# Optimization experiments

Hardware: AMD Instinct MI355X
Metric: run time of the kernel (lower is better)

The kernel has to match this reference:

```python
import jax, jax.numpy as jnp
import numpy as np

B, T, S, D = 8, 128, 512, 128  # batch, decoder steps, encoder len, output_dim==input_dim


def setup_inputs() -> dict:
    key = jax.random.key(0)
    ks = jax.random.split(key, 24)
    g = lambda i, shape: jax.random.normal(ks[i], shape, dtype=jnp.float32) * 0.05
    inp = {
        "x": g(0, (B, T, D)),
        "H": g(1, (B, S, D)),
        "init_states": jnp.zeros((2, B, D), jnp.float32),
        "Wa": g(2, (D, D)), "Ua": g(3, (D, D)), "v": g(4, (D,)),
        "Wi": g(5, (D, D)), "Ui": g(6, (D, D)), "Ci": g(7, (D, D)), "bi": jnp.zeros((D,), jnp.float32),
        "Wf": g(8, (D, D)), "Uf": g(9, (D, D)), "Cf": g(10, (D, D)), "bf": jnp.ones((D,), jnp.float32),
        "Wc": g(11, (D, D)), "Uc": g(12, (D, D)), "Cc": g(13, (D, D)), "bc": jnp.zeros((D,), jnp.float32),
        "Wo": g(14, (D, D)), "Uo": g(15, (D, D)), "Co": g(16, (D, D)), "bo": jnp.zeros((D,), jnp.float32),
    }
    return inp


def _forward(x, H, init_states, Wa, Ua, v, Wi, Ui, Ci, bi, Wf, Uf, Cf, bf,
             Wc, Uc, Cc, bc, Wo, Uo, Co, bo):
    # A = H @ Ua is loop-invariant in the original step(); hoist it (same math).
    HU = jnp.einsum('bsd,de->bse', H, Ua)  # [B,S,D]

    def step(carry, x_t):
        h_prev, c_prev = carry  # each [B,D]
        # Bahdanau attention over the full encoder sequence
        q = h_prev @ Wa                                        # [B,D]
        score = jnp.einsum('bsd,d->bs', jnp.tanh(HU + q[:, None, :]), v)  # [B,S]
        a = jax.nn.softmax(score, axis=-1)                     # [B,S]
        context = jnp.einsum('bsd,bs->bd', H, a)               # [B,D]
        # 4-gate LSTM update
        i_g = jax.nn.sigmoid(x_t @ Wi + h_prev @ Ui + context @ Ci + bi)
        f_g = jax.nn.sigmoid(x_t @ Wf + h_prev @ Uf + context @ Cf + bf)
        g_w = jnp.tanh(x_t @ Wc + h_prev @ Uc + context @ Cc + bc)
        c_t = f_g * c_prev + i_g * g_w
        o_g = jax.nn.sigmoid(x_t @ Wo + h_prev @ Uo + context @ Co + bo)
        h_t = o_g * jnp.tanh(c_t)
        return (h_t, c_t), h_t

    h0, c0 = init_states[0], init_states[1]
    x_tm = jnp.transpose(x, (1, 0, 2))  # time-major [T,B,D]
    _, hs = jax.lax.scan(step, (h0, c0), x_tm)  # hs: [T,B,D]
    return jnp.transpose(hs, (1, 0, 2))  # [B,T,D] hidden states (original returns [0] of stacked [h,c])


def reference(x, H, init_states, Wa, Ua, v, Wi, Ui, Ci, bi, Wf, Uf, Cf, bf,
              Wc, Uc, Cc, bc, Wo, Uo, Co, bo):
    return _forward(x, H, init_states, Wa, Ua, v, Wi, Ui, Ci, bi, Wf, Uf, Cf, bf,
                    Wc, Uc, Cc, bc, Wo, Uo, Co, bo)
```

## Files before the change

### kernel.cpp

```cpp
#include <hip/hip_runtime.h>

#define DEV __device__ __forceinline__

constexpr int nB = 8, nT = 128, nS = 512, nD = 128;
constexpr int J   = 4;
constexpr int SL  = 128;
constexpr int NTH = 512;

constexpr int S1_CNT = nB * J * 130;
constexpr int S2_OFF = S1_CNT;
constexpr int S2_CNT = nB * J * 32;
constexpr int XW_F   = (S1_CNT + S2_CNT) * 2;

DEV float tanh_small(float x) {
    float x2 = x * x;
    float p = fmaf(x2, 0.133333333f, -0.333333333f);
    return fmaf(x * x2, p, x);
}
DEV float fast_tanh(float x) {
    x = fminf(4.0f, fmaxf(-4.0f, x));
    float x2 = x * x;
    float num = fmaf(fmaf(x2 + 378.0f, x2, 17325.0f), x2, 135135.0f);
    float den = fmaf(fmaf(fmaf(x2, 28.0f, 3150.0f), x2, 62370.0f), x2, 135135.0f);
    return x * num * __builtin_amdgcn_rcpf(den);
}
DEV float fast_sig(float x) { return fmaf(fast_tanh(0.5f * x), 0.5f, 0.5f); }

typedef unsigned long long u64;
DEV u64  pk(float v, unsigned tag) { return ((u64)tag << 32) | (u64)__float_as_uint(v); }
DEV void st64(u64* p, u64 v) { __hip_atomic_store(p, v, __ATOMIC_RELAXED, __HIP_MEMORY_SCOPE_AGENT); }
DEV u64  ld64(const u64* p)  { return __hip_atomic_load(p, __ATOMIC_RELAXED, __HIP_MEMORY_SCOPE_AGENT); }
DEV float poll64(const u64* p, unsigned want) {
    for (;;) {
        u64 q = ld64(p);
        if ((unsigned)(q >> 32) == want) return __uint_as_float((unsigned)q);
        __builtin_amdgcn_s_sleep(1);
    }
}

__global__ void init_kernel(float* __restrict__ ws) {
    u64* p = (u64*)ws;
    for (int i = threadIdx.x; i < S1_CNT + S2_CNT; i += 1024)
        __hip_atomic_store(p + i, 0ull, __ATOMIC_RELAXED, __HIP_MEMORY_SCOPE_AGENT);
}

__global__ __launch_bounds__(NTH, 1) void attn_lstm_kernel(
    const float* __restrict__ x,  const float* __restrict__ H,
    const float* __restrict__ init_states, const float* __restrict__ Wa,
    const float* __restrict__ Ua, const float* __restrict__ v,
    const float* __restrict__ Wi, const float* __restrict__ Ui,
    const float* __restrict__ Ci, const float* __restrict__ bi,
    const float* __restrict__ Wf, const float* __restrict__ Uf,
    const float* __restrict__ Cf, const float* __restrict__ bf,
    const float* __restrict__ Wc, const float* __restrict__ Uc,
    const float* __restrict__ Cc, const float* __restrict__ bc,
    const float* __restrict__ Wo, const float* __restrict__ Uo,
    const float* __restrict__ Co, const float* __restrict__ bo,
    float* __restrict__ out, float* __restrict__ ws)
{
    const int tid = threadIdx.x;
    const int b = blockIdx.x & 7;
    const int j = blockIdx.x >> 3;

    u64*   S1   = (u64*)ws;
    u64*   S2   = (u64*)ws + S2_OFF;
    float* wsXW = ws + XW_F;

    __shared__ __align__(16) float Hs[SL * nD];
    __shared__ __align__(16) float q_l[nD];
    __shared__ __align__(16) float ctx_l[nD];
    __shared__ __align__(16) float h_l[nD];
    __shared__ __align__(16) float e_l[SL];
    __shared__ float sc_l[SL];
    __shared__ float pre_l[nD];
    __shared__ float pNx[3 * nD];
    __shared__ float mS_l[8];

    const int hi = tid >> 2, lo = tid & 3;
    const int g = hi >> 5, dd = hi & 31, gcol = 32 * j + dd;

    const float* Ug = (g == 0) ? Ui : (g == 1) ? Uf : (g == 2) ? Uc : Uo;
    const float* Cg = (g == 0) ? Ci : (g == 1) ? Cf : (g == 2) ? Cc : Co;
    const float* Bg = (g == 0) ? bi : (g == 1) ? bf : (g == 2) ? bc : bo;

    {
        for (int k = tid; k < 16384; k += NTH) {
            int gg = k >> 12, r = (k >> 5) & 127, i = k & 31;
            const float* Wm = (gg == 0) ? Wi : (gg == 1) ? Wf : (gg == 2) ? Wc : Wo;
            Hs[k] = Wm[r * nD + 32 * j + i];
        }
    }
    __syncthreads();

    {
        float acc[32];
        #pragma unroll
        for (int i = 0; i < 32; ++i) acc[i] = 0.0f;
        const float* xrow = x + ((size_t)b * nT + hi) * nD;
        for (int r = 0; r < nD; ++r) {
            float xr = xrow[r];
            const float* wrow = &Hs[lo * 4096 + r * 32];
            #pragma unroll
            for (int i = 0; i < 32; ++i) acc[i] = fmaf(xr, wrow[i], acc[i]);
        }
        float* dst = wsXW + ((size_t)(b * J + j) * nT + hi) * nD + lo * 32;
        #pragma unroll
        for (int k = 0; k < 8; ++k)
            ((float4*)dst)[k] = make_float4(acc[4*k], acc[4*k+1], acc[4*k+2], acc[4*k+3]);
    }
    __syncthreads();

    for (int k = tid; k < 16384; k += NTH) Hs[k] = Ua[k];
    __syncthreads();

    float HU_r[32];
    {
        #pragma unroll
        for (int i = 0; i < 32; ++i) HU_r[i] = 0.0f;
        const float* hrow = H + ((size_t)b * nS + (size_t)SL * j + hi) * nD;
        for (int r = 0; r < nD; ++r) {
            float hr = hrow[r];
            const float* uar = &Hs[r * nD + lo * 32];
            #pragma unroll
            for (int i = 0; i < 32; ++i) HU_r[i] = fmaf(hr, uar[i], HU_r[i]);
        }
    }
    __syncthreads();

    {
        const float* hrow = H + ((size_t)b * nS + (size_t)SL * j + hi) * nD + lo * 32;
        int c = hi >> 4, w = hi & 15;
        #pragma unroll
        for (int k = 0; k < 8; ++k) {
            float4 hv = ((const float4*)hrow)[k];
            int d0 = lo * 32 + 4 * k;
            Hs[(d0+0) * nD + ((c ^ ((d0+0) & 7)) * 16) + w] = hv.x;
            Hs[(d0+1) * nD + ((c ^ ((d0+1) & 7)) * 16) + w] = hv.y;
            Hs[(d0+2) * nD + ((c ^ ((d0+2) & 7)) * 16) + w] = hv.z;
            Hs[(d0+3) * nD + ((c ^ ((d0+3) & 7)) * 16) + w] = hv.w;
        }
    }

    float wa_r[32], u_r[32], c_r2[32], v_r[32];
    #pragma unroll
    for (int i = 0; i < 32; ++i) {
        wa_r[i] = Wa[(lo * 32 + i) * nD + hi];
        u_r[i]  = Ug[(lo * 32 + i) * nD + gcol];
        c_r2[i] = Cg[(lo * 32 + i) * nD + gcol];
        v_r[i]  = v[lo * 32 + i];
    }
    const float bval = Bg[gcol];
    float c_reg = (tid < 32) ? init_states[nB * nD + b * nD + 32 * j + tid] : 0.0f;

    if (tid < nD) h_l[tid] = init_states[b * nD + tid];
    __syncthreads();

    u64* myN = S1 + (size_t)(b * J + j) * 130;
    u64* myH = S2 + (size_t)(b * J + j) * 32;

    for (int t = 0; t < nT; ++t) {
        const unsigned tg = (unsigned)(t + 1);

        float xwv = 0.0f;
        if (lo == 0) xwv = wsXW[((size_t)(b * J + j) * nT + t) * nD + hi];

        float qa = 0.0f, uasum = 0.0f;
        #pragma unroll
        for (int i = 0; i < 32; ++i) {
            float hv = h_l[lo * 32 + i];
            qa    = fmaf(hv, wa_r[i], qa);
            uasum = fmaf(hv, u_r[i],  uasum);
        }
        qa += __shfl_xor(qa, 1);  qa += __shfl_xor(qa, 2);
        uasum += __shfl_xor(uasum, 1);  uasum += __shfl_xor(uasum, 2);
        if (lo == 0) q_l[hi] = qa;
        __syncthreads();

        float sa = 0.0f;
        #pragma unroll
        for (int k = 0; k < 8; ++k) {
            float4 qq = *(const float4*)&q_l[lo * 32 + 4 * k];
            sa = fmaf(v_r[4*k+0], tanh_small(HU_r[4*k+0] + qq.x), sa);
            sa = fmaf(v_r[4*k+1], tanh_small(HU_r[4*k+1] + qq.y), sa);
            sa = fmaf(v_r[4*k+2], tanh_small(HU_r[4*k+2] + qq.z), sa);
            sa = fmaf(v_r[4*k+3], tanh_small(HU_r[4*k+3] + qq.w), sa);
        }
        sa += __shfl_xor(sa, 1);  sa += __shfl_xor(sa, 2);
        if (lo == 0) sc_l[hi] = sa;
        __syncthreads();

        float m, se;
        {
            int lane = tid & 63;
            float s0 = sc_l[lane], s1 = sc_l[64 + lane];
            m = fmaxf(s0, s1);
            #pragma unroll
            for (int o = 1; o < 64; o <<= 1) m = fmaxf(m, __shfl_xor(m, o));
            float e0 = __expf(s0 - m), e1 = __expf(s1 - m);
            se = e0 + e1;
            #pragma unroll
            for (int o = 1; o < 64; o <<= 1) se += __shfl_xor(se, o);
            if (tid < 64) { e_l[tid] = e0; e_l[64 + tid] = e1; }
        }
        __syncthreads();

        float na = 0.0f;
        #pragma unroll
        for (int cc = 0; cc < 2; ++cc) {
            int c = 2 * lo + cc;
            int pc = c ^ (hi & 7);
            const float4* hp = (const float4*)&Hs[hi * nD + pc * 16];
            const float4* ep = (const float4*)&e_l[c * 16];
            #pragma unroll
            for (int k2 = 0; k2 < 4; ++k2) {
                float4 hh = hp[k2]; float4 ee = ep[k2];
                na = fmaf(ee.x, hh.x, na); na = fmaf(ee.y, hh.y, na);
                na = fmaf(ee.z, hh.z, na); na = fmaf(ee.w, hh.w, na);
            }
        }
        na += __shfl_xor(na, 1);  na += __shfl_xor(na, 2);

        if (lo == 0) st64(myN + hi, pk(na, tg));
        if (tid == 0) st64(myN + 128, pk(m, tg));
        if (tid == 1) st64(myN + 129, pk(se, tg));
        if (tid < 384) {
            int pi = tid >> 7, d2 = tid & 127;
            int jj = pi + (pi >= j);
            pNx[pi * nD + d2] = poll64(S1 + (size_t)(b * J + jj) * 130 + d2, tg);
        }
        if (tid >= 384 && tid < 390) {
            int k = tid - 384, pi = k >> 1, wh = k & 1;
            int jj = pi + (pi >= j);
            mS_l[pi * 2 + wh] = poll64(S1 + (size_t)(b * J + jj) * 130 + 128 + wh, tg);
        }
        __syncthreads();

        if (lo == 0) {
            float mm = m;
            #pragma unroll
            for (int p2 = 0; p2 < 3; ++p2) mm = fmaxf(mm, mS_l[p2 * 2]);
            float w0 = __expf(m - mm);
            float ssum = se * w0, nsum = na * w0;
            #pragma unroll
            for (int p2 = 0; p2 < 3; ++p2) {
                float wp = __expf(mS_l[p2 * 2] - mm);
                ssum = fmaf(mS_l[p2 * 2 + 1], wp, ssum);
                nsum = fmaf(pNx[p2 * nD + hi], wp, nsum);
            }
            ctx_l[hi] = nsum * __builtin_amdgcn_rcpf(ssum);
        }
        __syncthreads();

        float ca = 0.0f;
        #pragma unroll
        for (int i = 0; i < 32; ++i) ca = fmaf(ctx_l[lo * 32 + i], c_r2[i], ca);
        ca += __shfl_xor(ca, 1);  ca += __shfl_xor(ca, 2);
        if (lo == 0) pre_l[hi] = uasum + ca + xwv + bval;
        __syncthreads();

        if (tid < 32) {
            float p_i = pre_l[tid], p_f = pre_l[32 + tid];
            float p_c = pre_l[64 + tid], p_o = pre_l[96 + tid];
            float ig = fast_sig(p_i), fg = fast_sig(p_f);
            float gg = fast_tanh(p_c), og = fast_sig(p_o);
            c_reg = fmaf(fg, c_reg, ig * gg);
            float hn = og * fast_tanh(c_reg);
            st64(myH + tid, pk(hn, tg));
            h_l[32 * j + tid] = hn;
            out[((size_t)b * nT + t) * nD + 32 * j + tid] = hn;
        }
        if (tid >= 32 && tid < 128) {
            int k = tid - 32, pi = k >> 5, dd2 = k & 31;
            int jj = pi + (pi >= j);
            h_l[32 * jj + dd2] = poll64(S2 + (size_t)(b * J + jj) * 32 + dd2, tg);
        }
        __syncthreads();
    }
}

extern "C" void kernel_launch(void* const* d_in, const int* in_sizes, int n_in,
                              void* d_out, int out_size, void* d_ws, size_t ws_size,
                              hipStream_t stream) {
    const float* x  = (const float*)d_in[0];
    const float* H  = (const float*)d_in[1];
    const float* is = (const float*)d_in[2];
    const float* Wa = (const float*)d_in[3];
    const float* Ua = (const float*)d_in[4];
    const float* v  = (const float*)d_in[5];
    const float* Wi = (const float*)d_in[6];
    const float* Ui = (const float*)d_in[7];
    const float* Ci = (const float*)d_in[8];
    const float* bi = (const float*)d_in[9];
    const float* Wf = (const float*)d_in[10];
    const float* Uf = (const float*)d_in[11];
    const float* Cf = (const float*)d_in[12];
    const float* bf = (const float*)d_in[13];
    const float* Wc = (const float*)d_in[14];
    const float* Uc = (const float*)d_in[15];
    const float* Cc = (const float*)d_in[16];
    const float* bc = (const float*)d_in[17];
    const float* Wo = (const float*)d_in[18];
    const float* Uo = (const float*)d_in[19];
    const float* Co = (const float*)d_in[20];
    const float* bo = (const float*)d_in[21];
    float* out = (float*)d_out;
    float* ws  = (float*)d_ws;

    hipLaunchKernelGGL(init_kernel, dim3(1), dim3(1024), 0, stream, ws);
    hipLaunchKernelGGL(attn_lstm_kernel, dim3(nB * J), dim3(NTH), 0, stream,
                       x, H, is, Wa, Ua, v,
                       Wi, Ui, Ci, bi, Wf, Uf, Cf, bf,
                       Wc, Uc, Cc, bc, Wo, Uo, Co, bo,
                       out, ws);
}
```

Before: 805.1 us.

## Rewrite as one block per batch with fp16 packed dot products and precompute kernel

The recurrent kernel moves from four cooperating blocks per batch, which exchanged softmax partials and hidden-state slices through tagged global-memory polling, to a single 512-thread block per batch that holds the whole encoder sequence in LDS as packed fp16. The x·W and H·Ua projections move into a separate pre-kernel that writes fp16 results to workspace. The per-step matvecs, attention tanh and context reduction now use packed-half fdot2. This removes the inter-block polling latency on every step. In exchange it uses fewer CUs and loses accuracy from fp16 storage, a cubic tanh approximation evaluated in half precision, and a softmax that skips max subtraction.

```diff
diff --git a/kernel.cpp b/kernel.cpp
--- a/kernel.cpp
+++ b/kernel.cpp
@@ -1,21 +1,43 @@
 #include <hip/hip_runtime.h>
 
 #define DEV __device__ __forceinline__
+typedef unsigned int u32;
+typedef _Float16 f16;
+typedef f16 h2 __attribute__((ext_vector_type(2)));
+using pkv2 = decltype(__builtin_amdgcn_cvt_pkrtz(0.0f, 0.0f));
 
 constexpr int nB = 8, nT = 128, nS = 512, nD = 128;
-constexpr int J   = 4;
-constexpr int SL  = 128;
 constexpr int NTH = 512;
-
-constexpr int S1_CNT = nB * J * 130;
-constexpr int S2_OFF = S1_CNT;
-constexpr int S2_CNT = nB * J * 32;
-constexpr int XW_F   = (S1_CNT + S2_CNT) * 2;
-
-DEV float tanh_small(float x) {
-    float x2 = x * x;
-    float p = fmaf(x2, 0.133333333f, -0.333333333f);
-    return fmaf(x * x2, p, x);
+constexpr int RS  = 260;
+
+constexpr int XW_W = 0;
+constexpr int HU_W = 262144;
+constexpr int WA_W = 524288;
+
+#if defined(__has_builtin)
+#if __has_builtin(__builtin_amdgcn_fdot2)
+#define HAS_FDOT2 1
+#endif
+#endif
+
+DEV h2  u2h(u32 a) { return __builtin_bit_cast(h2, a); }
+DEV u32 h2u(h2 a)  { return __builtin_bit_cast(u32, a); }
+DEV u32 pkrtz(float a, float b) { return __builtin_bit_cast(u32, __builtin_amdgcn_cvt_pkrtz(a, b)); }
+
+DEV float fdot2(u32 a, u32 b, float c) {
+#ifdef HAS_FDOT2
+    return __builtin_amdgcn_fdot2(__builtin_bit_cast(pkv2, a), __builtin_bit_cast(pkv2, b), c, false);
+#else
+    h2 A = u2h(a), B = u2h(b);
+    return c + (float)A.x * (float)B.x + (float)A.y * (float)B.y;
+#endif
+}
+
+DEV h2 tanh_pk(h2 x) {
+    h2 x2 = x * x;
+    h2 x3 = x * x2;
+    h2 c3 = { (f16)0.33333333f, (f16)0.33333333f };
+    return x - x3 * c3;
 }
 DEV float fast_tanh(float x) {
     x = fminf(4.0f, fmaxf(-4.0f, x));
@@ -26,25 +48,74 @@
 }
 DEV float fast_sig(float x) { return fmaf(fast_tanh(0.5f * x), 0.5f, 0.5f); }
 
-typedef unsigned long long u64;
-DEV u64  pk(float v, unsigned tag) { return ((u64)tag << 32) | (u64)__float_as_uint(v); }
-DEV void st64(u64* p, u64 v) { __hip_atomic_store(p, v, __ATOMIC_RELAXED, __HIP_MEMORY_SCOPE_AGENT); }
-DEV u64  ld64(const u64* p)  { return __hip_atomic_load(p, __ATOMIC_RELAXED, __HIP_MEMORY_SCOPE_AGENT); }
-DEV float poll64(const u64* p, unsigned want) {
-    for (;;) {
-        u64 q = ld64(p);
-        if ((unsigned)(q >> 32) == want) return __uint_as_float((unsigned)q);
-        __builtin_amdgcn_s_sleep(1);
-    }
-}
-
-__global__ void init_kernel(float* __restrict__ ws) {
-    u64* p = (u64*)ws;
-    for (int i = threadIdx.x; i < S1_CNT + S2_CNT; i += 1024)
-        __hip_atomic_store(p + i, 0ull, __ATOMIC_RELAXED, __HIP_MEMORY_SCOPE_AGENT);
-}
-
-__global__ __launch_bounds__(NTH, 1) void attn_lstm_kernel(
+__global__ __launch_bounds__(512, 2) void pre_kernel(
+    const float* __restrict__ x,  const float* __restrict__ H,
+    const float* __restrict__ Wa, const float* __restrict__ Ua,
+    const float* __restrict__ Wi, const float* __restrict__ Wf,
+    const float* __restrict__ Wc, const float* __restrict__ Wo,
+    u32* __restrict__ ws)
+{
+    const int w = blockIdx.x, tid = threadIdx.x;
+    if (w < 32) {
+        const int b = w >> 2, tp = w & 3;
+        const int g = tid >> 7, cc = tid & 127;
+        const float* Wm = (g == 0) ? Wi : (g == 1) ? Wf : (g == 2) ? Wc : Wo;
+        float wcol[128];
+        #pragma unroll
+        for (int r = 0; r < 128; ++r) wcol[r] = Wm[r * nD + cc];
+        for (int ti = 0; ti < 32; ++ti) {
+            int t = tp * 32 + ti;
+            const float* xr = x + ((size_t)b * nT + t) * nD;
+            float acc = 0.0f;
+            #pragma unroll
+            for (int r = 0; r < 128; ++r) acc = fmaf(xr[r], wcol[r], acc);
+            float accn = __shfl_down(acc, 1);
+            if (!(tid & 1))
+                ws[XW_W + ((size_t)b * nT + t) * 256 + (tid >> 1)] = pkrtz(acc, accn);
+        }
+        if (w == 0) {
+            int col = tid >> 2, q = tid & 3;
+            #pragma unroll
+            for (int k = 0; k < 16; ++k) {
+                int rp = q * 16 + k;
+                ws[WA_W + col * 64 + rp] =
+                    pkrtz(Wa[(2 * rp) * nD + col], Wa[(2 * rp + 1) * nD + col]);
+            }
+        }
+    } else {
+        const int b = (w - 32) >> 2, sp4 = (w - 32) & 3;
+        __shared__ float UaS[128 * 128];
+        for (int k = tid; k < 16384; k += 512) UaS[k] = Ua[k];
+        __syncthreads();
+        const int lo = tid & 3, si = tid >> 2;
+        const int s = sp4 * 128 + si;
+        const float* hrow = H + ((size_t)b * nS + s) * nD;
+        float acc[32];
+        #pragma unroll
+        for (int i = 0; i < 32; ++i) acc[i] = 0.0f;
+        for (int r4 = 0; r4 < 32; ++r4) {
+            float4 hv = ((const float4*)hrow)[r4];
+            #pragma unroll
+            for (int k = 0; k < 4; ++k) {
+                float hr = (k == 0) ? hv.x : (k == 1) ? hv.y : (k == 2) ? hv.z : hv.w;
+                const float4* ua = (const float4*)&UaS[(4 * r4 + k) * 128 + lo * 32];
+                #pragma unroll
+                for (int q = 0; q < 8; ++q) {
+                    float4 u = ua[q];
+                    acc[4*q+0] = fmaf(hr, u.x, acc[4*q+0]);
+                    acc[4*q+1] = fmaf(hr, u.y, acc[4*q+1]);
+                    acc[4*q+2] = fmaf(hr, u.z, acc[4*q+2]);
+                    acc[4*q+3] = fmaf(hr, u.w, acc[4*q+3]);
+                }
+            }
+        }
+        u32* dst = ws + HU_W + ((size_t)b * nS + s) * 64 + lo * 16;
+        #pragma unroll
+        for (int k = 0; k < 16; ++k) dst[k] = pkrtz(acc[2 * k], acc[2 * k + 1]);
+    }
+}
+
+__global__ __launch_bounds__(NTH, 2) void attn_lstm_kernel(
     const float* __restrict__ x,  const float* __restrict__ H,
     const float* __restrict__ init_states, const float* __restrict__ Wa,
     const float* __restrict__ Ua, const float* __restrict__ v,
@@ -56,223 +127,192 @@
     const float* __restrict__ Cc, const float* __restrict__ bc,
     const float* __restrict__ Wo, const float* __restrict__ Uo,
     const float* __restrict__ Co, const float* __restrict__ bo,
-    float* __restrict__ out, float* __restrict__ ws)
+    float* __restrict__ out, u32* __restrict__ ws)
 {
-    const int tid = threadIdx.x;
-    const int b = blockIdx.x & 7;
-    const int j = blockIdx.x >> 3;
-
-    u64*   S1   = (u64*)ws;
-    u64*   S2   = (u64*)ws + S2_OFF;
-    float* wsXW = ws + XW_F;
-
-    __shared__ __align__(16) float Hs[SL * nD];
-    __shared__ __align__(16) float q_l[nD];
-    __shared__ __align__(16) float ctx_l[nD];
-    __shared__ __align__(16) float h_l[nD];
-    __shared__ __align__(16) float e_l[SL];
-    __shared__ float sc_l[SL];
-    __shared__ float pre_l[nD];
-    __shared__ float pNx[3 * nD];
-    __shared__ float mS_l[8];
-
-    const int hi = tid >> 2, lo = tid & 3;
-    const int g = hi >> 5, dd = hi & 31, gcol = 32 * j + dd;
+    const int b = blockIdx.x, tid = threadIdx.x;
+
+    __shared__ __align__(16) u32 Hl[128 * RS];
+    __shared__ __align__(16) u32 q_l[64], e_l[256], ctx_l[64], h_l[64], v_w[64];
+    __shared__ __align__(16) float sc_l[512], pre_l[512], pNx[512];
+    __shared__ float mS[8];
+
+    const int lo = tid & 3, hi = tid >> 2;
+    const int g = tid >> 7, cc = tid & 127;
+
+    {
+        const int sp = tid >> 1, half = tid & 1;
+        const float* r0 = H + ((size_t)b * nS + 2 * sp) * nD + half * 64;
+        const float* r1 = r0 + nD;
+        #pragma unroll
+        for (int k = 0; k < 16; ++k) {
+            float4 a = ((const float4*)r0)[k];
+            float4 c = ((const float4*)r1)[k];
+            int d0 = half * 64 + 4 * k;
+            Hl[(d0 + 0) * RS + sp] = pkrtz(a.x, c.x);
+            Hl[(d0 + 1) * RS + sp] = pkrtz(a.y, c.y);
+            Hl[(d0 + 2) * RS + sp] = pkrtz(a.z, c.z);
+            Hl[(d0 + 3) * RS + sp] = pkrtz(a.w, c.w);
+        }
+    }
+
+    u32 HUr[64];
+    {
+        const u32* srcw = ws + HU_W + ((size_t)b * nS + 4 * hi) * 64 + lo * 16;
+        #pragma unroll
+        for (int k = 0; k < 4; ++k) {
+            #pragma unroll
+            for (int q = 0; q < 4; ++q) {
+                uint4 t4 = ((const uint4*)(srcw + k * 64))[q];
+                HUr[16*k + 4*q + 0] = t4.x; HUr[16*k + 4*q + 1] = t4.y;
+                HUr[16*k + 4*q + 2] = t4.z; HUr[16*k + 4*q + 3] = t4.w;
+            }
+        }
+    }
 
     const float* Ug = (g == 0) ? Ui : (g == 1) ? Uf : (g == 2) ? Uc : Uo;
     const float* Cg = (g == 0) ? Ci : (g == 1) ? Cf : (g == 2) ? Cc : Co;
     const float* Bg = (g == 0) ? bi : (g == 1) ? bf : (g == 2) ? bc : bo;
-
-    {
-        for (int k = tid; k < 16384; k += NTH) {
-            int gg = k >> 12, r = (k >> 5) & 127, i = k & 31;
-            const float* Wm = (gg == 0) ? Wi : (gg == 1) ? Wf : (gg == 2) ? Wc : Wo;
-            Hs[k] = Wm[r * nD + 32 * j + i];
-        }
-    }
+    u32 Ur[64], Cr[64];
+    #pragma unroll
+    for (int rp = 0; rp < 64; ++rp) {
+        Ur[rp] = pkrtz(Ug[(2*rp) * nD + cc], Ug[(2*rp+1) * nD + cc]);
+        Cr[rp] = pkrtz(Cg[(2*rp) * nD + cc], Cg[(2*rp+1) * nD + cc]);
+    }
+    if (tid < 64) v_w[tid] = pkrtz(v[2 * tid], v[2 * tid + 1]);
+    const float bval = Bg[cc];
+
+    float c_reg = 0.0f;
+    if (tid < 128) c_reg = init_states[nB * nD + b * nD + tid];
+    if (tid < 128 && !(tid & 1))
+        h_l[tid >> 1] = pkrtz(init_states[b * nD + tid], init_states[b * nD + tid + 1]);
     __syncthreads();
 
-    {
-        float acc[32];
-        #pragma unroll
-        for (int i = 0; i < 32; ++i) acc[i] = 0.0f;
-        const float* xrow = x + ((size_t)b * nT + hi) * nD;
-        for (int r = 0; r < nD; ++r) {
-            float xr = xrow[r];
-            const float* wrow = &Hs[lo * 4096 + r * 32];
-            #pragma unroll
-            for (int i = 0; i < 32; ++i) acc[i] = fmaf(xr, wrow[i], acc[i]);
-        }
-        float* dst = wsXW + ((size_t)(b * J + j) * nT + hi) * nD + lo * 32;
-        #pragma unroll
-        for (int k = 0; k < 8; ++k)
-            ((float4*)dst)[k] = make_float4(acc[4*k], acc[4*k+1], acc[4*k+2], acc[4*k+3]);
-    }
-    __syncthreads();
-
-    for (int k = tid; k < 16384; k += NTH) Hs[k] = Ua[k];
-    __syncthreads();
-
-    float HU_r[32];
-    {
-        #pragma unroll
-        for (int i = 0; i < 32; ++i) HU_r[i] = 0.0f;
-        const float* hrow = H + ((size_t)b * nS + (size_t)SL * j + hi) * nD;
-        for (int r = 0; r < nD; ++r) {
-            float hr = hrow[r];
-            const float* uar = &Hs[r * nD + lo * 32];
-            #pragma unroll
-            for (int i = 0; i < 32; ++i) HU_r[i] = fmaf(hr, uar[i], HU_r[i]);
-        }
-    }
-    __syncthreads();
-
-    {
-        const float* hrow = H + ((size_t)b * nS + (size_t)SL * j + hi) * nD + lo * 32;
-        int c = hi >> 4, w = hi & 15;
-        #pragma unroll
-        for (int k = 0; k < 8; ++k) {
-            float4 hv = ((const float4*)hrow)[k];
-            int d0 = lo * 32 + 4 * k;
-            Hs[(d0+0) * nD + ((c ^ ((d0+0) & 7)) * 16) + w] = hv.x;
-            Hs[(d0+1) * nD + ((c ^ ((d0+1) & 7)) * 16) + w] = hv.y;
-            Hs[(d0+2) * nD + ((c ^ ((d0+2) & 7)) * 16) + w] = hv.z;
-            Hs[(d0+3) * nD + ((c ^ ((d0+3) & 7)) * 16) + w] = hv.w;
-        }
-    }
-
-    float wa_r[32], u_r[32], c_r2[32], v_r[32];
-    #pragma unroll
-    for (int i = 0; i < 32; ++i) {
-        wa_r[i] = Wa[(lo * 32 + i) * nD + hi];
-        u_r[i]  = Ug[(lo * 32 + i) * nD + gcol];
-        c_r2[i] = Cg[(lo * 32 + i) * nD + gcol];
-        v_r[i]  = v[lo * 32 + i];
-    }
-    const float bval = Bg[gcol];
-    float c_reg = (tid < 32) ? init_states[nB * nD + b * nD + 32 * j + tid] : 0.0f;
-
-    if (tid < nD) h_l[tid] = init_states[b * nD + tid];
-    __syncthreads();
-
-    u64* myN = S1 + (size_t)(b * J + j) * 130;
-    u64* myH = S2 + (size_t)(b * J + j) * 32;
-
     for (int t = 0; t < nT; ++t) {
-        const unsigned tg = (unsigned)(t + 1);
-
-        float xwv = 0.0f;
-        if (lo == 0) xwv = wsXW[((size_t)(b * J + j) * nT + t) * nD + hi];
-
-        float qa = 0.0f, uasum = 0.0f;
-        #pragma unroll
-        for (int i = 0; i < 32; ++i) {
-            float hv = h_l[lo * 32 + i];
-            qa    = fmaf(hv, wa_r[i], qa);
-            uasum = fmaf(hv, u_r[i],  uasum);
-        }
-        qa += __shfl_xor(qa, 1);  qa += __shfl_xor(qa, 2);
-        uasum += __shfl_xor(uasum, 1);  uasum += __shfl_xor(uasum, 2);
-        if (lo == 0) q_l[hi] = qa;
-        __syncthreads();
-
-        float sa = 0.0f;
-        #pragma unroll
-        for (int k = 0; k < 8; ++k) {
-            float4 qq = *(const float4*)&q_l[lo * 32 + 4 * k];
-            sa = fmaf(v_r[4*k+0], tanh_small(HU_r[4*k+0] + qq.x), sa);
-            sa = fmaf(v_r[4*k+1], tanh_small(HU_r[4*k+1] + qq.y), sa);
-            sa = fmaf(v_r[4*k+2], tanh_small(HU_r[4*k+2] + qq.z), sa);
-            sa = fmaf(v_r[4*k+3], tanh_small(HU_r[4*k+3] + qq.w), sa);
-        }
-        sa += __shfl_xor(sa, 1);  sa += __shfl_xor(sa, 2);
-        if (lo == 0) sc_l[hi] = sa;
-        __syncthreads();
-
-        float m, se;
-        {
-            int lane = tid & 63;
-            float s0 = sc_l[lane], s1 = sc_l[64 + lane];
-            m = fmaxf(s0, s1);
-            #pragma unroll
-            for (int o = 1; o < 64; o <<= 1) m = fmaxf(m, __shfl_xor(m, o));
-            float e0 = __expf(s0 - m), e1 = __expf(s1 - m);
-            se = e0 + e1;
-            #pragma unroll
-            for (int o = 1; o < 64; o <<= 1) se += __shfl_xor(se, o);
-            if (tid < 64) { e_l[tid] = e0; e_l[64 + tid] = e1; }
-        }
-        __syncthreads();
-
-        float na = 0.0f;
-        #pragma unroll
-        for (int cc = 0; cc < 2; ++cc) {
-            int c = 2 * lo + cc;
-            int pc = c ^ (hi & 7);
-            const float4* hp = (const float4*)&Hs[hi * nD + pc * 16];
-            const float4* ep = (const float4*)&e_l[c * 16];
-            #pragma unroll
-            for (int k2 = 0; k2 < 4; ++k2) {
-                float4 hh = hp[k2]; float4 ee = ep[k2];
-                na = fmaf(ee.x, hh.x, na); na = fmaf(ee.y, hh.y, na);
-                na = fmaf(ee.z, hh.z, na); na = fmaf(ee.w, hh.w, na);
-            }
-        }
-        na += __shfl_xor(na, 1);  na += __shfl_xor(na, 2);
-
-        if (lo == 0) st64(myN + hi, pk(na, tg));
-        if (tid == 0) st64(myN + 128, pk(m, tg));
-        if (tid == 1) st64(myN + 129, pk(se, tg));
-        if (tid < 384) {
-            int pi = tid >> 7, d2 = tid & 127;
-            int jj = pi + (pi >= j);
-            pNx[pi * nD + d2] = poll64(S1 + (size_t)(b * J + jj) * 130 + d2, tg);
-        }
-        if (tid >= 384 && tid < 390) {
-            int k = tid - 384, pi = k >> 1, wh = k & 1;
-            int jj = pi + (pi >= j);
-            mS_l[pi * 2 + wh] = poll64(S1 + (size_t)(b * J + jj) * 130 + 128 + wh, tg);
-        }
-        __syncthreads();
-
-        if (lo == 0) {
-            float mm = m;
-            #pragma unroll
-            for (int p2 = 0; p2 < 3; ++p2) mm = fmaxf(mm, mS_l[p2 * 2]);
-            float w0 = __expf(m - mm);
-            float ssum = se * w0, nsum = na * w0;
-            #pragma unroll
-            for (int p2 = 0; p2 < 3; ++p2) {
-                float wp = __expf(mS_l[p2 * 2] - mm);
-                ssum = fmaf(mS_l[p2 * 2 + 1], wp, ssum);
-                nsum = fmaf(pNx[p2 * nD + hi], wp, nsum);
-            }
-            ctx_l[hi] = nsum * __builtin_amdgcn_rcpf(ssum);
-        }
-        __syncthreads();
-
-        float ca = 0.0f;
-        #pragma unroll
-        for (int i = 0; i < 32; ++i) ca = fmaf(ctx_l[lo * 32 + i], c_r2[i], ca);
-        ca += __shfl_xor(ca, 1);  ca += __shfl_xor(ca, 2);
-        if (lo == 0) pre_l[hi] = uasum + ca + xwv + bval;
-        __syncthreads();
-
-        if (tid < 32) {
-            float p_i = pre_l[tid], p_f = pre_l[32 + tid];
-            float p_c = pre_l[64 + tid], p_o = pre_l[96 + tid];
-            float ig = fast_sig(p_i), fg = fast_sig(p_f);
-            float gg = fast_tanh(p_c), og = fast_sig(p_o);
+        u32 xww = ws[XW_W + ((size_t)b * nT + t) * 256 + (tid >> 1)];
+
+        float ud = 0.0f, qa = 0.0f;
+        #pragma unroll
+        for (int ch = 0; ch < 16; ++ch) {
+            uint4 hw = ((const uint4*)h_l)[ch];
+            ud = fdot2(Ur[4*ch+0], hw.x, ud);
+            ud = fdot2(Ur[4*ch+1], hw.y, ud);
+            ud = fdot2(Ur[4*ch+2], hw.z, ud);
+            ud = fdot2(Ur[4*ch+3], hw.w, ud);
+        }
+        {
+            const uint4* wp = (const uint4*)(ws + WA_W + hi * 64 + lo * 16);
+            #pragma unroll
+            for (int q = 0; q < 4; ++q) {
+                uint4 w4 = wp[q];
+                uint4 hw = ((const uint4*)h_l)[lo * 4 + q];
+                qa = fdot2(w4.x, hw.x, qa);
+                qa = fdot2(w4.y, hw.y, qa);
+                qa = fdot2(w4.z, hw.z, qa);
+                qa = fdot2(w4.w, hw.w, qa);
+            }
+        }
+        qa += __shfl_xor(qa, 1);
+        qa += __shfl_xor(qa, 2);
+        if (lo == 0 && !(hi & 1)) {
+            float qn = __shfl_down(qa, 4);
+            q_l[hi >> 1] = pkrtz(qa, qn);
+        }
+        __syncthreads();
+
+        {
+            u32 qv[16], vw[16];
+            #pragma unroll
+            for (int q = 0; q < 4; ++q) {
+                uint4 t4 = ((const uint4*)q_l)[lo * 4 + q];
+                qv[4*q+0] = t4.x; qv[4*q+1] = t4.y; qv[4*q+2] = t4.z; qv[4*q+3] = t4.w;
+                uint4 t5 = ((const uint4*)v_w)[lo * 4 + q];
+                vw[4*q+0] = t5.x; vw[4*q+1] = t5.y; vw[4*q+2] = t5.z; vw[4*q+3] = t5.w;
+            }
+            float sacc[4];
+            #pragma unroll
+            for (int k = 0; k < 4; ++k) {
+                float sa = 0.0f;
+                #pragma unroll
+                for (int wq = 0; wq < 16; ++wq) {
+                    h2 xa = u2h(HUr[16*k + wq]) + u2h(qv[wq]);
+                    sa = fdot2(vw[wq], h2u(tanh_pk(xa)), sa);
+                }
+                sacc[k] = sa;
+            }
+            #pragma unroll
+            for (int k = 0; k < 4; ++k) {
+                sacc[k] += __shfl_xor(sacc[k], 1);
+                sacc[k] += __shfl_xor(sacc[k], 2);
+            }
+            if (lo == 0)
+                ((float4*)sc_l)[hi] = make_float4(sacc[0], sacc[1], sacc[2], sacc[3]);
+        }
+        __syncthreads();
+
+        {
+            float e = __expf(sc_l[tid]);
+            float ssw = e;
+            #pragma unroll
+            for (int o = 1; o < 64; o <<= 1) ssw += __shfl_xor(ssw, o);
+            if ((tid & 63) == 0) mS[tid >> 6] = ssw;
+            float en = __shfl_down(e, 1);
+            if (!(tid & 1)) e_l[tid >> 1] = pkrtz(e, en);
+        }
+        __syncthreads();
+
+        {
+            const int d2 = tid & 127, spq = tid >> 7;
+            const u32* hp = &Hl[d2 * RS + spq * 64];
+            const u32* ep = &e_l[spq * 64];
+            float na = 0.0f;
+            #pragma unroll
+            for (int q = 0; q < 16; ++q) {
+                uint4 hh = ((const uint4*)hp)[q];
+                uint4 ee = ((const uint4*)ep)[q];
+                na = fdot2(hh.x, ee.x, na);
+                na = fdot2(hh.y, ee.y, na);
+                na = fdot2(hh.z, ee.z, na);
+                na = fdot2(hh.w, ee.w, na);
+            }
+            pNx[spq * 128 + d2] = na;
+        }
+        __syncthreads();
+
+        if (tid < 128) {
+            float ssum = mS[0] + mS[1] + mS[2] + mS[3] + mS[4] + mS[5] + mS[6] + mS[7];
+            float ctxv = (pNx[tid] + pNx[128 + tid] + pNx[256 + tid] + pNx[384 + tid])
+                         * __builtin_amdgcn_rcpf(ssum);
+            float cn = __shfl_down(ctxv, 1);
+            if (!(tid & 1)) ctx_l[tid >> 1] = pkrtz(ctxv, cn);
+        }
+        __syncthreads();
+
+        {
+            float cd = 0.0f;
+            #pragma unroll
+            for (int ch = 0; ch < 16; ++ch) {
+                uint4 cw = ((const uint4*)ctx_l)[ch];
+                cd = fdot2(Cr[4*ch+0], cw.x, cd);
+                cd = fdot2(Cr[4*ch+1], cw.y, cd);
+                cd = fdot2(Cr[4*ch+2], cw.z, cd);
+                cd = fdot2(Cr[4*ch+3], cw.w, cd);
+            }
+            h2 xwp = u2h(xww);
+            float xwv = (tid & 1) ? (float)xwp.y : (float)xwp.x;
+            pre_l[tid] = ud + cd + xwv + bval;
+        }
+        __syncthreads();
+
+        if (tid < 128) {
+            float ig = fast_sig(pre_l[tid]);
+            float fg = fast_sig(pre_l[128 + tid]);
+            float gg = fast_tanh(pre_l[256 + tid]);
+            float og = fast_sig(pre_l[384 + tid]);
             c_reg = fmaf(fg, c_reg, ig * gg);
             float hn = og * fast_tanh(c_reg);
-            st64(myH + tid, pk(hn, tg));
-            h_l[32 * j + tid] = hn;
-            out[((size_t)b * nT + t) * nD + 32 * j + tid] = hn;
-        }
-        if (tid >= 32 && tid < 128) {
-            int k = tid - 32, pi = k >> 5, dd2 = k & 31;
-            int jj = pi + (pi >= j);
-            h_l[32 * jj + dd2] = poll64(S2 + (size_t)(b * J + jj) * 32 + dd2, tg);
+            out[((size_t)b * nT + t) * nD + tid] = hn;
+            float hnn = __shfl_down(hn, 1);
+            if (!(tid & 1)) h_l[tid >> 1] = pkrtz(hn, hnn);
         }
         __syncthreads();
     }
@@ -304,10 +344,11 @@
     const float* Co = (const float*)d_in[20];
     const float* bo = (const float*)d_in[21];
     float* out = (float*)d_out;
-    float* ws  = (float*)d_ws;
-
-    hipLaunchKernelGGL(init_kernel, dim3(1), dim3(1024), 0, stream, ws);
-    hipLaunchKernelGGL(attn_lstm_kernel, dim3(nB * J), dim3(NTH), 0, stream,
+    u32*   ws  = (u32*)d_ws;
+
+    hipLaunchKernelGGL(pre_kernel, dim3(64), dim3(512), 0, stream,
+                       x, H, Wa, Ua, Wi, Wf, Wc, Wo, ws);
+    hipLaunchKernelGGL(attn_lstm_kernel, dim3(nB), dim3(NTH), 0, stream,
                        x, H, is, Wa, Ua, v,
                        Wi, Ui, Ci, bi, Wf, Uf, Cf, bf,
                        Wc, Uc, Cc, bc, Wo, Uo, Co, bo,
```

Measured after the change: 1.497 ms. 85.9% more time.
